# Optimization experiments

Measured on AMD Instinct MI355X. Metric: run time of the kernel, lower is better.

The kernel has to match this reference:

```python
import jax, jax.numpy as jnp
import numpy as np

N_POINTS = 4
HIDDEN = 128


def _grid_sample(features, grid):
    """Bilinear grid_sample, align_corners=True, zero padding.
    features: [B, C, H, W]; grid: [B, J, P, 2] with (x, y) in [-1, 1].
    Returns [B, C, J, P]."""
    B, C, H, W = features.shape
    ix = (grid[..., 0] + 1.0) * 0.5 * (W - 1)  # [B,J,P]
    iy = (grid[..., 1] + 1.0) * 0.5 * (H - 1)
    x0 = jnp.floor(ix); y0 = jnp.floor(iy)
    x1 = x0 + 1.0;      y1 = y0 + 1.0
    wx1 = ix - x0; wx0 = 1.0 - wx1
    wy1 = iy - y0; wy0 = 1.0 - wy1

    def corner(xf, yf):
        valid = (xf >= 0) & (xf <= W - 1) & (yf >= 0) & (yf <= H - 1)
        xi = jnp.clip(xf, 0, W - 1).astype(jnp.int32)
        yi = jnp.clip(yf, 0, H - 1).astype(jnp.int32)

        def gather_one(fb, yb, xb, vb):
            # fb: [C,H,W]; yb, xb, vb: [J,P]
            return fb[:, yb, xb] * vb[None].astype(fb.dtype)  # [C,J,P]

        return jax.vmap(gather_one)(features, yi, xi, valid)

    v00 = corner(x0, y0); v01 = corner(x1, y0)
    v10 = corner(x0, y1); v11 = corner(x1, y1)
    w00 = (wx0 * wy0)[:, None]  # [B,1,J,P]
    w01 = (wx1 * wy0)[:, None]
    w10 = (wx0 * wy1)[:, None]
    w11 = (wx1 * wy1)[:, None]
    return v00 * w00 + v01 * w01 + v10 * w10 + v11 * w11


def _mlp1x1(x, w1, b1, w2, b2):
    # 1x1 conv stack on [B, C, J] points: Conv(C->128) -> ReLU -> Conv(128->O)
    h = jax.nn.relu(jnp.einsum('oc,bcj->boj', w1, x) + b1[None, :, None])
    return jnp.einsum('oc,bcj->boj', w2, h) + b2[None, :, None]


def setup_inputs() -> dict:
    key = jax.random.key(0)
    ks = jax.random.split(key, 12)
    B, C, H, W, J = 32, 1024, 64, 64, 128
    features = jax.random.normal(ks[0], (B, C, H, W), dtype=jnp.float32)
    keypoint_coords = jax.random.uniform(ks[1], (B, J, 2), dtype=jnp.float32,
                                         minval=-1.0, maxval=1.0)
    # offset predictor params (small std so predicted pixel offsets stay local)
    w_off1 = jax.random.normal(ks[2], (HIDDEN, C), dtype=jnp.float32) * 0.01
    b_off1 = jax.random.normal(ks[3], (HIDDEN,), dtype=jnp.float32) * 0.01
    w_off2 = jax.random.normal(ks[4], (2 * N_POINTS, HIDDEN), dtype=jnp.float32) * 0.01
    b_off2 = jax.random.normal(ks[5], (2 * N_POINTS,), dtype=jnp.float32) * 0.01
    # attention predictor params
    w_att1 = jax.random.normal(ks[6], (HIDDEN, C), dtype=jnp.float32) * 0.02
    b_att1 = jax.random.normal(ks[7], (HIDDEN,), dtype=jnp.float32) * 0.02
    w_att2 = jax.random.normal(ks[8], (N_POINTS, HIDDEN), dtype=jnp.float32) * 0.02
    b_att2 = jax.random.normal(ks[9], (N_POINTS,), dtype=jnp.float32) * 0.02
    return {"features": features, "keypoint_coords": keypoint_coords,
            "w_off1": w_off1, "b_off1": b_off1, "w_off2": w_off2, "b_off2": b_off2,
            "w_att1": w_att1, "b_att1": b_att1, "w_att2": w_att2, "b_att2": b_att2}


def reference(features, keypoint_coords, w_off1, b_off1, w_off2, b_off2,
              w_att1, b_att1, w_att2, b_att2):
    B, C, H, W = features.shape
    J = keypoint_coords.shape[1]
    # seed features at keypoints: [B, C, J]
    seed = _grid_sample(features, keypoint_coords[:, :, None, :])[..., 0]
    offsets = _mlp1x1(seed, w_off1, b_off1, w_off2, b_off2)      # [B, 2N, J]
    attn_logits = _mlp1x1(seed, w_att1, b_att1, w_att2, b_att2)  # [B, N, J]
    # [B, 2N, J] -> [B, J, N, 2]; channel pairs are (x, y) per point
    off = offsets.transpose(0, 2, 1).reshape(B, J, N_POINTS, 2)
    scale = jnp.array([2.0 / (W - 1), 2.0 / (H - 1)], dtype=features.dtype)
    new_grid = keypoint_coords[:, :, None, :] + off * scale       # [B, J, N, 2]
    sampled = _grid_sample(features, new_grid)                    # [B, C, J, N]
    attw = jax.nn.softmax(attn_logits.transpose(0, 2, 1), axis=-1)  # [B, J, N]
    fused = jnp.einsum('bcjn,bjn->bjc', sampled, attw)            # [B, J, C]
    return fused
```

## Files before the change

### kernel.cpp

```cpp
#include <hip/hip_runtime.h>
#include <math.h>

#define BB  32
#define CCH 1024
#define HH  64
#define WW  64
#define JJ  128
#define NP  4
#define HID 128

typedef float f4 __attribute__((ext_vector_type(4)));
typedef __attribute__((ext_vector_type(8))) short bf8_t;
typedef __attribute__((ext_vector_type(4))) float f32x4;
typedef __attribute__((ext_vector_type(4))) unsigned short us4;

__device__ __forceinline__ unsigned short f2bf(float x) {
  union { float f; unsigned int u; } v; v.f = x;
  unsigned int u = v.u;
  return (unsigned short)((u + 0x7FFFu + ((u >> 16) & 1u)) >> 16);
}

__device__ __forceinline__ float bilin(const float* pl, float ix, float iy) {
  float x0f = floorf(ix), y0f = floorf(iy);
  float wx1 = ix - x0f, wx0 = 1.0f - wx1;
  float wy1 = iy - y0f, wy0 = 1.0f - wy1;
  int x0 = (int)x0f, y0 = (int)y0f;
  int x1 = x0 + 1, y1 = y0 + 1;
  float v = 0.0f;
  if (y0 >= 0 && y0 < HH) {
    if (x0 >= 0 && x0 < WW) v += pl[y0*WW + x0] * (wx0*wy0);
    if (x1 >= 0 && x1 < WW) v += pl[y0*WW + x1] * (wx1*wy0);
  }
  if (y1 >= 0 && y1 < HH) {
    if (x0 >= 0 && x0 < WW) v += pl[y1*WW + x0] * (wx0*wy1);
    if (x1 >= 0 && x1 < WW) v += pl[y1*WW + x1] * (wx1*wy1);
  }
  return v;
}

__global__ __launch_bounds__(256) void k_prep(const float* __restrict__ w_off1,
                                              const float* __restrict__ w_att1,
                                              unsigned short* __restrict__ Wb) {
  int o = blockIdx.x, m = blockIdx.y;
  const float* src = (m ? w_att1 : w_off1) + (size_t)o * CCH;
  unsigned short* dst = Wb + ((size_t)m * HID + o) * CCH;
  int t = threadIdx.x;
  f4 v = *(const f4*)&src[t * 4];
  us4 u; u[0] = f2bf(v[0]); u[1] = f2bf(v[1]); u[2] = f2bf(v[2]); u[3] = f2bf(v[3]);
  *(us4*)&dst[t * 4] = u;
}

__global__ __launch_bounds__(256) void k_seed(const float* __restrict__ feat,
                                              const float* __restrict__ kp,
                                              unsigned short* __restrict__ seedB) {
  int c = blockIdx.x, b = blockIdx.y;
  __shared__ __align__(16) float pl[HH*WW];
  const f4* p4 = (const f4*)(feat + ((size_t)(b*CCH + c)) * (size_t)(HH*WW));
  f4* s4 = (f4*)pl;
  #pragma unroll
  for (int r = 0; r < 4; ++r) s4[threadIdx.x + r*256] = p4[threadIdx.x + r*256];
  __syncthreads();
  int j = threadIdx.x;
  if (j < JJ) {
    float gx = kp[((size_t)b*JJ + j)*2 + 0];
    float gy = kp[((size_t)b*JJ + j)*2 + 1];
    float ix = (gx + 1.0f) * 0.5f * (float)(WW - 1);
    float iy = (gy + 1.0f) * 0.5f * (float)(HH - 1);
    seedB[((size_t)(b*CCH + c))*JJ + j] = f2bf(bilin(pl, ix, iy));
  }
}

__global__ __launch_bounds__(256) void k_str(const unsigned short* __restrict__ seedB,
                                             unsigned short* __restrict__ seedT) {
  int c0 = blockIdx.x * 32, j0 = blockIdx.y * 32, b = blockIdx.z;
  __shared__ unsigned short tl[32][34];
  int tx = threadIdx.x & 31, ty = threadIdx.x >> 5;
  #pragma unroll
  for (int r = 0; r < 4; ++r)
    tl[ty + r*8][tx] = seedB[((size_t)(b*CCH + c0 + ty + r*8))*JJ + j0 + tx];
  __syncthreads();
  #pragma unroll
  for (int r = 0; r < 4; ++r) {
    int jr = ty + r*8;
    seedT[((size_t)b*JJ + j0 + jr)*CCH + c0 + tx] = tl[tx][jr];
  }
}

__global__ __launch_bounds__(256) void k_mlp2(const unsigned short* __restrict__ seedT,
                                              const unsigned short* __restrict__ Wb,
                                              const float* __restrict__ b_off1,
                                              const float* __restrict__ b_att1,
                                              float* __restrict__ hidden) {
  int m = blockIdx.x, b = blockIdx.y;
  __shared__ __align__(16) unsigned short sA[128][72];
  __shared__ __align__(16) unsigned short sB[128][72];
  int t = threadIdx.x;
  int w = t >> 6, l = t & 63;
  int lr = l & 15, lg = l >> 4;
  f32x4 acc[2][8];
  #pragma unroll
  for (int jt = 0; jt < 2; ++jt)
    #pragma unroll
    for (int ot = 0; ot < 8; ++ot) acc[jt][ot] = (f32x4)0.0f;

  const unsigned short* At = seedT + (size_t)b * JJ * CCH;
  const unsigned short* Bt = Wb + (size_t)m * HID * CCH;

  for (int kc = 0; kc < 16; ++kc) {
    int k0 = kc * 64;
    #pragma unroll
    for (int q = 0; q < 4; ++q) {
      int idx = q * 256 + t;
      int r = idx >> 3, s = idx & 7;
      *(bf8_t*)&sA[r][s*8] = *(const bf8_t*)&At[(size_t)r*CCH + k0 + s*8];
      *(bf8_t*)&sB[r][s*8] = *(const bf8_t*)&Bt[(size_t)r*CCH + k0 + s*8];
    }
    __syncthreads();
    #pragma unroll
    for (int ks = 0; ks < 2; ++ks) {
      int koff = ks*32 + lg*8;
      bf8_t a0 = *(const bf8_t*)&sA[w*32 + lr][koff];
      bf8_t a1 = *(const bf8_t*)&sA[w*32 + 16 + lr][koff];
      #pragma unroll
      for (int ot = 0; ot < 8; ++ot) {
        bf8_t bb = *(const bf8_t*)&sB[ot*16 + lr][koff];
        acc[0][ot] = __builtin_amdgcn_mfma_f32_16x16x32_bf16(a0, bb, acc[0][ot], 0, 0, 0);
        acc[1][ot] = __builtin_amdgcn_mfma_f32_16x16x32_bf16(a1, bb, acc[1][ot], 0, 0, 0);
      }
    }
    __syncthreads();
  }

  const float* bias = m ? b_att1 : b_off1;
  float* Hb = hidden + ((size_t)b * 2 + m) * JJ * HID;
  #pragma unroll
  for (int jt = 0; jt < 2; ++jt) {
    #pragma unroll
    for (int ot = 0; ot < 8; ++ot) {
      int o = ot*16 + lr;
      float bo = bias[o];
      #pragma unroll
      for (int r = 0; r < 4; ++r) {
        int j = w*32 + jt*16 + lg*4 + r;
        Hb[(size_t)j*HID + o] = fmaxf(acc[jt][ot][r] + bo, 0.0f);
      }
    }
  }
}

__global__ __launch_bounds__(256) void k_head2(const float* __restrict__ hidden,
                                               const float* __restrict__ kp,
                                               const float* __restrict__ w_off2,
                                               const float* __restrict__ b_off2,
                                               const float* __restrict__ w_att2,
                                               const float* __restrict__ b_att2,
                                               float* __restrict__ grids,
                                               float* __restrict__ attw) {
  int jq = blockIdx.x, b = blockIdx.y;
  int j0 = jq * 32;
  __shared__ __align__(16) float sH[2][32][132];
  __shared__ float sO[32][13];
  int t = threadIdx.x;
  for (int idx = t; idx < 2048; idx += 256) {
    int m = idx >> 10, rem = idx & 1023;
    int jl = rem >> 5, oq = rem & 31;
    *(f4*)&sH[m][jl][oq*4] =
        *(const f4*)&hidden[(((size_t)b*2 + m)*JJ + j0 + jl)*HID + oq*4];
  }
  __syncthreads();
  for (int idx = t; idx < 12*32; idx += 256) {
    int jl = idx / 12, q = idx % 12;
    int m = (q < 8) ? 0 : 1;
    int p = m ? (q - 8) : q;
    const float* w2 = m ? w_att2 : w_off2;
    float sum = (m ? b_att2 : b_off2)[p];
    for (int o = 0; o < HID; ++o) sum += w2[p*HID + o] * sH[m][jl][o];
    sO[jl][q] = sum;
  }
  __syncthreads();
  if (t < 32) {
    int jl = t, j = j0 + jl;
    float gx = kp[((size_t)b*JJ + j)*2 + 0];
    float gy = kp[((size_t)b*JJ + j)*2 + 1];
    const float sc = 2.0f / 63.0f;
    float a[NP];
    #pragma unroll
    for (int n = 0; n < NP; ++n) {
      grids[(((size_t)b*JJ + j)*NP + n)*2 + 0] = gx + sO[jl][2*n + 0]*sc;
      grids[(((size_t)b*JJ + j)*NP + n)*2 + 1] = gy + sO[jl][2*n + 1]*sc;
      a[n] = sO[jl][8 + n];
    }
    float mx = fmaxf(fmaxf(a[0], a[1]), fmaxf(a[2], a[3]));
    float e[NP], s = 0.0f;
    #pragma unroll
    for (int n = 0; n < NP; ++n) { e[n] = expf(a[n] - mx); s += e[n]; }
    float inv = 1.0f / s;
    #pragma unroll
    for (int n = 0; n < NP; ++n) attw[((size_t)b*JJ + j)*NP + n] = e[n]*inv;
  }
}

__global__ __launch_bounds__(256) void k_fuse2(const float* __restrict__ feat,
                                               const float* __restrict__ grids,
                                               const float* __restrict__ attw,
                                               float* __restrict__ out) {
  int c0 = blockIdx.x * 16, b = blockIdx.y;
  __shared__ __align__(16) float plane[2][HH*WW];
  __shared__ float sT[JJ][17];
  __shared__ float sG[JJ*NP*2];
  __shared__ float sAw[JJ*NP];
  int t = threadIdx.x;
  const f4* gb = (const f4*)(grids + (size_t)b*JJ*NP*2);
  const f4* ab = (const f4*)(attw  + (size_t)b*JJ*NP);
  ((f4*)sG)[t] = gb[t];
  if (t < 128) ((f4*)sAw)[t] = ab[t];

  const float* base = feat + ((size_t)(b*CCH + c0)) * (size_t)(HH*WW);
  f4 r[4];
  {
    const f4* p0 = (const f4*)base;
    #pragma unroll
    for (int q = 0; q < 4; ++q) r[q] = p0[t + q*256];
    f4* d = (f4*)plane[0];
    #pragma unroll
    for (int q = 0; q < 4; ++q) d[t + q*256] = r[q];
  }
  __syncthreads();

  for (int i = 0; i < 16; ++i) {
    int cur = i & 1;
    if (i < 15) {
      const f4* pn = (const f4*)(base + (size_t)(i + 1) * (HH*WW));
      #pragma unroll
      for (int q = 0; q < 4; ++q) r[q] = pn[t + q*256];
    }
    if (t < JJ) {
      float acc = 0.0f;
      #pragma unroll
      for (int n = 0; n < NP; ++n) {
        float gx = sG[(t*NP + n)*2 + 0];
        float gy = sG[(t*NP + n)*2 + 1];
        float ix = (gx + 1.0f) * 0.5f * (float)(WW - 1);
        float iy = (gy + 1.0f) * 0.5f * (float)(HH - 1);
        acc += sAw[t*NP + n] * bilin(plane[cur], ix, iy);
      }
      sT[t][i] = acc;
    }
    __syncthreads();
    if (i < 15) {
      f4* d = (f4*)plane[cur ^ 1];
      #pragma unroll
      for (int q = 0; q < 4; ++q) d[t + q*256] = r[q];
    }
    __syncthreads();
  }

  if (t < JJ) {
    f4* dst = (f4*)&out[((size_t)b*JJ + t)*CCH + c0];
    #pragma unroll
    for (int q = 0; q < 4; ++q) {
      f4 v;
      v[0] = sT[t][q*4 + 0]; v[1] = sT[t][q*4 + 1];
      v[2] = sT[t][q*4 + 2]; v[3] = sT[t][q*4 + 3];
      dst[q] = v;
    }
  }
}

extern "C" void kernel_launch(void* const* d_in, const int* in_sizes, int n_in,
                              void* d_out, int out_size, void* d_ws, size_t ws_size,
                              hipStream_t stream) {
  const float* feat   = (const float*)d_in[0];
  const float* kp     = (const float*)d_in[1];
  const float* w_off1 = (const float*)d_in[2];
  const float* b_off1 = (const float*)d_in[3];
  const float* w_off2 = (const float*)d_in[4];
  const float* b_off2 = (const float*)d_in[5];
  const float* w_att1 = (const float*)d_in[6];
  const float* b_att1 = (const float*)d_in[7];
  const float* w_att2 = (const float*)d_in[8];
  const float* b_att2 = (const float*)d_in[9];
  float* out = (float*)d_out;

  float* ws = (float*)d_ws;
  float*          grids = ws;
  float*          attwb = ws + (size_t)32768;
  unsigned short* Wb    = (unsigned short*)(ws + (size_t)49152);
  unsigned short* seedB = (unsigned short*)(ws + (size_t)180224);
  unsigned short* seedT = (unsigned short*)(ws + (size_t)2277376);
  float*          hid   = ws + (size_t)4374528;

  k_prep <<<dim3(HID, 2), 256, 0, stream>>>(w_off1, w_att1, Wb);
  k_seed <<<dim3(CCH, BB), 256, 0, stream>>>(feat, kp, seedB);
  k_str  <<<dim3(CCH/32, JJ/32, BB), 256, 0, stream>>>(seedB, seedT);
  k_mlp2 <<<dim3(2, BB), 256, 0, stream>>>(seedT, Wb, b_off1, b_att1, hid);
  k_head2<<<dim3(4, BB), 256, 0, stream>>>(hid, kp, w_off2, b_off2, w_att2, b_att2,
                                           grids, attwb);
  k_fuse2<<<dim3(CCH/16, BB), 256, 0, stream>>>(feat, grids, attwb, out);
}
```

Before: 245.7 us.

## Fuse seed sampling with transpose, fold weight bf16 cast into MLP, single-buffer planes

Replaces the separate seed-sampling and transpose kernels with one kernel. It streams 16 channel planes per block and writes the transposed bf16 seed directly, and it drops the weight-prep kernel by converting fp32 weights to bf16 inside the MLP tile load. The fuse kernel moves from a double-buffered plane to a single buffer in LDS. Its grid coordinates and attention weights now live in registers instead of shared memory, which lowers LDS use and may raise occupancy. The trade-offs are extra fp32 weight traffic and conversion work repeated in each MLP block, plus a second barrier on every iteration.

```diff
diff --git a/kernel.cpp b/kernel.cpp
--- a/kernel.cpp
+++ b/kernel.cpp
@@ -38,56 +38,65 @@
   return v;
 }
 
-__global__ __launch_bounds__(256) void k_prep(const float* __restrict__ w_off1,
+__global__ __launch_bounds__(256) void k_seedT(const float* __restrict__ feat,
+                                               const float* __restrict__ kp,
+                                               unsigned short* __restrict__ seedT) {
+  int c0 = blockIdx.x * 16, b = blockIdx.y;
+  __shared__ __align__(16) float plane[HH*WW];
+  __shared__ float sT[JJ][17];
+  int t = threadIdx.x;
+
+  float ix = 0.0f, iy = 0.0f;
+  if (t < JJ) {
+    float gx = kp[((size_t)b*JJ + t)*2 + 0];
+    float gy = kp[((size_t)b*JJ + t)*2 + 1];
+    ix = (gx + 1.0f) * 0.5f * (float)(WW - 1);
+    iy = (gy + 1.0f) * 0.5f * (float)(HH - 1);
+  }
+
+  const float* base = feat + ((size_t)(b*CCH + c0)) * (size_t)(HH*WW);
+  f4 r[4];
+  {
+    const f4* p0 = (const f4*)base;
+    #pragma unroll
+    for (int q = 0; q < 4; ++q) r[q] = p0[t + q*256];
+    f4* d = (f4*)plane;
+    #pragma unroll
+    for (int q = 0; q < 4; ++q) d[t + q*256] = r[q];
+  }
+  __syncthreads();
+
+  for (int i = 0; i < 16; ++i) {
+    if (i < 15) {
+      const f4* pn = (const f4*)(base + (size_t)(i + 1) * (HH*WW));
+      #pragma unroll
+      for (int q = 0; q < 4; ++q) r[q] = pn[t + q*256];
+    }
+    if (t < JJ) sT[t][i] = bilin(plane, ix, iy);
+    __syncthreads();
+    if (i < 15) {
+      f4* d = (f4*)plane;
+      #pragma unroll
+      for (int q = 0; q < 4; ++q) d[t + q*256] = r[q];
+      __syncthreads();
+    }
+  }
+
+  if (t < JJ) {
+    unsigned short* dst = &seedT[((size_t)b*JJ + t)*CCH + c0];
+    #pragma unroll
+    for (int q = 0; q < 4; ++q) {
+      us4 u;
+      u[0] = f2bf(sT[t][q*4 + 0]); u[1] = f2bf(sT[t][q*4 + 1]);
+      u[2] = f2bf(sT[t][q*4 + 2]); u[3] = f2bf(sT[t][q*4 + 3]);
+      *(us4*)&dst[q*4] = u;
+    }
+  }
+}
+
+__global__ __launch_bounds__(256) void k_mlp2(const unsigned short* __restrict__ seedT,
+                                              const float* __restrict__ w_off1,
                                               const float* __restrict__ w_att1,
-                                              unsigned short* __restrict__ Wb) {
-  int o = blockIdx.x, m = blockIdx.y;
-  const float* src = (m ? w_att1 : w_off1) + (size_t)o * CCH;
-  unsigned short* dst = Wb + ((size_t)m * HID + o) * CCH;
-  int t = threadIdx.x;
-  f4 v = *(const f4*)&src[t * 4];
-  us4 u; u[0] = f2bf(v[0]); u[1] = f2bf(v[1]); u[2] = f2bf(v[2]); u[3] = f2bf(v[3]);
-  *(us4*)&dst[t * 4] = u;
-}
-
-__global__ __launch_bounds__(256) void k_seed(const float* __restrict__ feat,
-                                              const float* __restrict__ kp,
-                                              unsigned short* __restrict__ seedB) {
-  int c = blockIdx.x, b = blockIdx.y;
-  __shared__ __align__(16) float pl[HH*WW];
-  const f4* p4 = (const f4*)(feat + ((size_t)(b*CCH + c)) * (size_t)(HH*WW));
-  f4* s4 = (f4*)pl;
-  #pragma unroll
-  for (int r = 0; r < 4; ++r) s4[threadIdx.x + r*256] = p4[threadIdx.x + r*256];
-  __syncthreads();
-  int j = threadIdx.x;
-  if (j < JJ) {
-    float gx = kp[((size_t)b*JJ + j)*2 + 0];
-    float gy = kp[((size_t)b*JJ + j)*2 + 1];
-    float ix = (gx + 1.0f) * 0.5f * (float)(WW - 1);
-    float iy = (gy + 1.0f) * 0.5f * (float)(HH - 1);
-    seedB[((size_t)(b*CCH + c))*JJ + j] = f2bf(bilin(pl, ix, iy));
-  }
-}
-
-__global__ __launch_bounds__(256) void k_str(const unsigned short* __restrict__ seedB,
-                                             unsigned short* __restrict__ seedT) {
-  int c0 = blockIdx.x * 32, j0 = blockIdx.y * 32, b = blockIdx.z;
-  __shared__ unsigned short tl[32][34];
-  int tx = threadIdx.x & 31, ty = threadIdx.x >> 5;
-  #pragma unroll
-  for (int r = 0; r < 4; ++r)
-    tl[ty + r*8][tx] = seedB[((size_t)(b*CCH + c0 + ty + r*8))*JJ + j0 + tx];
-  __syncthreads();
-  #pragma unroll
-  for (int r = 0; r < 4; ++r) {
-    int jr = ty + r*8;
-    seedT[((size_t)b*JJ + j0 + jr)*CCH + c0 + tx] = tl[tx][jr];
-  }
-}
-
-__global__ __launch_bounds__(256) void k_mlp2(const unsigned short* __restrict__ seedT,
-                                              const unsigned short* __restrict__ Wb,
                                               const float* __restrict__ b_off1,
                                               const float* __restrict__ b_att1,
                                               float* __restrict__ hidden) {
@@ -104,7 +113,7 @@
     for (int ot = 0; ot < 8; ++ot) acc[jt][ot] = (f32x4)0.0f;
 
   const unsigned short* At = seedT + (size_t)b * JJ * CCH;
-  const unsigned short* Bt = Wb + (size_t)m * HID * CCH;
+  const float* Wt = m ? w_att1 : w_off1;
 
   for (int kc = 0; kc < 16; ++kc) {
     int k0 = kc * 64;
@@ -113,7 +122,15 @@
       int idx = q * 256 + t;
       int r = idx >> 3, s = idx & 7;
       *(bf8_t*)&sA[r][s*8] = *(const bf8_t*)&At[(size_t)r*CCH + k0 + s*8];
-      *(bf8_t*)&sB[r][s*8] = *(const bf8_t*)&Bt[(size_t)r*CCH + k0 + s*8];
+    }
+    #pragma unroll
+    for (int q = 0; q < 8; ++q) {
+      int idx = q * 256 + t;
+      int r = idx >> 4, s = idx & 15;
+      f4 v = *(const f4*)&Wt[(size_t)r*CCH + k0 + s*4];
+      us4 u;
+      u[0] = f2bf(v[0]); u[1] = f2bf(v[1]); u[2] = f2bf(v[2]); u[3] = f2bf(v[3]);
+      *(us4*)&sB[r][s*4] = u;
     }
     __syncthreads();
     #pragma unroll
@@ -205,15 +222,21 @@
                                                const float* __restrict__ attw,
                                                float* __restrict__ out) {
   int c0 = blockIdx.x * 16, b = blockIdx.y;
-  __shared__ __align__(16) float plane[2][HH*WW];
+  __shared__ __align__(16) float plane[HH*WW];
   __shared__ float sT[JJ][17];
-  __shared__ float sG[JJ*NP*2];
-  __shared__ float sAw[JJ*NP];
   int t = threadIdx.x;
-  const f4* gb = (const f4*)(grids + (size_t)b*JJ*NP*2);
-  const f4* ab = (const f4*)(attw  + (size_t)b*JJ*NP);
-  ((f4*)sG)[t] = gb[t];
-  if (t < 128) ((f4*)sAw)[t] = ab[t];
+
+  float ixr[NP], iyr[NP], awr[NP];
+  if (t < JJ) {
+    #pragma unroll
+    for (int n = 0; n < NP; ++n) {
+      float gx = grids[(((size_t)b*JJ + t)*NP + n)*2 + 0];
+      float gy = grids[(((size_t)b*JJ + t)*NP + n)*2 + 1];
+      ixr[n] = (gx + 1.0f) * 0.5f * (float)(WW - 1);
+      iyr[n] = (gy + 1.0f) * 0.5f * (float)(HH - 1);
+      awr[n] = attw[((size_t)b*JJ + t)*NP + n];
+    }
+  }
 
   const float* base = feat + ((size_t)(b*CCH + c0)) * (size_t)(HH*WW);
   f4 r[4];
@@ -221,14 +244,13 @@
     const f4* p0 = (const f4*)base;
     #pragma unroll
     for (int q = 0; q < 4; ++q) r[q] = p0[t + q*256];
-    f4* d = (f4*)plane[0];
+    f4* d = (f4*)plane;
     #pragma unroll
     for (int q = 0; q < 4; ++q) d[t + q*256] = r[q];
   }
   __syncthreads();
 
   for (int i = 0; i < 16; ++i) {
-    int cur = i & 1;
     if (i < 15) {
       const f4* pn = (const f4*)(base + (size_t)(i + 1) * (HH*WW));
       #pragma unroll
@@ -237,22 +259,16 @@
     if (t < JJ) {
       float acc = 0.0f;
       #pragma unroll
-      for (int n = 0; n < NP; ++n) {
-        float gx = sG[(t*NP + n)*2 + 0];
-        float gy = sG[(t*NP + n)*2 + 1];
-        float ix = (gx + 1.0f) * 0.5f * (float)(WW - 1);
-        float iy = (gy + 1.0f) * 0.5f * (float)(HH - 1);
-        acc += sAw[t*NP + n] * bilin(plane[cur], ix, iy);
-      }
+      for (int n = 0; n < NP; ++n) acc += awr[n] * bilin(plane, ixr[n], iyr[n]);
       sT[t][i] = acc;
     }
     __syncthreads();
     if (i < 15) {
-      f4* d = (f4*)plane[cur ^ 1];
+      f4* d = (f4*)plane;
       #pragma unroll
       for (int q = 0; q < 4; ++q) d[t + q*256] = r[q];
-    }
-    __syncthreads();
+      __syncthreads();
+    }
   }
 
   if (t < JJ) {
@@ -285,15 +301,11 @@
   float* ws = (float*)d_ws;
   float*          grids = ws;
   float*          attwb = ws + (size_t)32768;
-  unsigned short* Wb    = (unsigned short*)(ws + (size_t)49152);
-  unsigned short* seedB = (unsigned short*)(ws + (size_t)180224);
-  unsigned short* seedT = (unsigned short*)(ws + (size_t)2277376);
-  float*          hid   = ws + (size_t)4374528;
-
-  k_prep <<<dim3(HID, 2), 256, 0, stream>>>(w_off1, w_att1, Wb);
-  k_seed <<<dim3(CCH, BB), 256, 0, stream>>>(feat, kp, seedB);
-  k_str  <<<dim3(CCH/32, JJ/32, BB), 256, 0, stream>>>(seedB, seedT);
-  k_mlp2 <<<dim3(2, BB), 256, 0, stream>>>(seedT, Wb, b_off1, b_att1, hid);
+  unsigned short* seedT = (unsigned short*)(ws + (size_t)49152);
+  float*          hid   = ws + (size_t)2146304;
+
+  k_seedT<<<dim3(CCH/16, BB), 256, 0, stream>>>(feat, kp, seedT);
+  k_mlp2 <<<dim3(2, BB), 256, 0, stream>>>(seedT, w_off1, w_att1, b_off1, b_att1, hid);
   k_head2<<<dim3(4, BB), 256, 0, stream>>>(hid, kp, w_off2, b_off2, w_att2, b_att2,
                                            grids, attwb);
   k_fuse2<<<dim3(CCH/16, BB), 256, 0, stream>>>(feat, grids, attwb, out);
```

Result: slower. 253.6 us (+3.2%).
